# Kernel optimization log

Hardware: AMD Instinct MI355X
Metric: run time of the kernel (lower is better)

Reference implementation:

```python
import jax, jax.numpy as jnp
import numpy as np
from jax import lax

# norse LIF/LI default parameters
DT = 0.001
TAU_SYN_INV = 200.0   # 1/5e-3
TAU_MEM_INV = 100.0   # 1/1e-2
V_TH = 1.0
V_LEAK = 0.0
V_RESET = 0.0
ALPHA = 100.0         # SuperSpike surrogate slope (method='super')
SEQ_LEN = 40          # LIFConstantCurrentEncoder(40)
SCALE = 50.0

@jax.custom_vjp
def heaviside(x):
    # forward: spike if x > 0; backward: SuperSpike surrogate
    return (x > 0).astype(x.dtype)

def _h_fwd(x):
    return (x > 0).astype(x.dtype), x

def _h_bwd(x, g):
    return (g / (ALPHA * jnp.abs(x) + 1.0) ** 2,)

heaviside.defvjp(_h_fwd, _h_bwd)

def constant_current_encode(current):
    # LIF membrane driven by a constant input current; emit spike train (T, B, F)
    def step(v, _):
        v = v + DT * TAU_MEM_INV * ((V_LEAK - v) + current)
        z = heaviside(v - V_TH)
        v = (1.0 - z) * v  # reset to zero on spike
        return v, z
    _, spikes = lax.scan(step, jnp.zeros_like(current), None, length=SEQ_LEN)
    return spikes

def setup_inputs() -> dict:
    key = jax.random.key(0)
    k1, k2, k3, k4 = jax.random.split(key, 4)
    batch, state_dim, hidden, out = 65536, 4, 128, 2
    x = jax.random.normal(k1, (batch, state_dim), jnp.float32)
    s_in = np.float32(np.sqrt(1.0 / (2 * state_dim)))
    s_hid = np.float32(np.sqrt(1.0 / hidden))
    w_in = jax.random.normal(k2, (hidden, 2 * state_dim), jnp.float32) * s_in   # LIFCell input weights
    w_rec = jax.random.normal(k3, (hidden, hidden), jnp.float32) * s_hid        # LIFCell recurrent weights
    w_out = jax.random.normal(k4, (out, hidden), jnp.float32) * s_hid           # LICell readout weights
    return {"x": x, "w_in": w_in, "w_rec": w_rec, "w_out": w_out}

def reference(x, w_in, w_rec, w_out):
    # encode positive / negative parts of the (scaled) observation into spikes
    x_pos = constant_current_encode(jax.nn.relu(SCALE * x))   # (T, B, 4)
    x_neg = constant_current_encode(jax.nn.relu(-SCALE * x))  # (T, B, 4)
    spikes = jnp.concatenate([x_pos, x_neg], axis=2)          # (T, B, 8)

    B = x.shape[0]
    H = w_in.shape[0]
    O = w_out.shape[0]
    z0 = jnp.zeros((B, H), x.dtype)
    v0 = jnp.zeros((B, H), x.dtype)
    i0 = jnp.zeros((B, H), x.dtype)
    vo0 = jnp.zeros((B, O), x.dtype)
    io0 = jnp.zeros((B, O), x.dtype)

    def step(carry, xt):
        z, v, i, vo, io = carry
        # --- LIFCell (recurrent spiking layer) ---
        i_dec = i - DT * TAU_SYN_INV * i
        v_dec = v + DT * TAU_MEM_INV * ((V_LEAK - v) + i)
        z_new = heaviside(v_dec - V_TH)
        v_new = (1.0 - z_new) * v_dec + z_new * V_RESET
        i_new = i_dec + xt @ w_in.T + z @ w_rec.T
        # dropout(p=0.5) is identity in eval mode
        # --- LICell (leaky-integrator readout) ---
        vo_new = vo + DT * TAU_MEM_INV * ((V_LEAK - vo) + io)
        io_new = io - DT * TAU_SYN_INV * io + z_new @ w_out.T
        return (z_new, v_new, i_new, vo_new, io_new), vo_new

    _, voltages = lax.scan(step, (z0, v0, i0, vo0, io0), spikes)  # (T, B, 2)
    m = jnp.max(voltages, axis=0)
    return jax.nn.softmax(m, axis=1)
```

## Files before the change

### kernel.cpp

```cpp
#include <hip/hip_runtime.h>


#pragma clang fp contract(off)

typedef float f32x4 __attribute__((ext_vector_type(4)));
typedef float f32x2 __attribute__((ext_vector_type(2)));
typedef short short8 __attribute__((ext_vector_type(8)));
typedef int int4v __attribute__((ext_vector_type(4)));

constexpr int TSTEPS = 40;

__device__ __forceinline__ unsigned rnbf(float f) {
    unsigned u = __float_as_uint(f);
    return (u + 0x7FFFu + ((u >> 16) & 1u)) & 0xFFFF0000u;
}

__device__ __forceinline__ void split2pair(float a, float b,
                                           unsigned& hi, unsigned& mi) {
    unsigned ha = rnbf(a), hb = rnbf(b);
    float ra = a - __uint_as_float(ha);
    float rb = b - __uint_as_float(hb);
    unsigned ma = rnbf(ra), mb = rnbf(rb);
    hi = (ha >> 16) | (hb & 0xFFFF0000u);
    mi = (ma >> 16) | (mb & 0xFFFF0000u);
}

__device__ __forceinline__ f32x4 mfma16(int4v a, int4v b, f32x4 c) {
    return __builtin_amdgcn_mfma_f32_16x16x32_bf16(
        __builtin_bit_cast(short8, a), __builtin_bit_cast(short8, b), c, 0, 0, 0);
}

template <int CTRL>
__device__ __forceinline__ float dpp_mov(float v) {
    return __int_as_float(
        __builtin_amdgcn_update_dpp(0, __float_as_int(v), CTRL, 0xF, 0xF, true));
}

__device__ __forceinline__ f32x2 lo2(f32x4 a) {
    return __builtin_shufflevector(a, a, 0, 1);
}
__device__ __forceinline__ f32x2 hi2(f32x4 a) {
    return __builtin_shufflevector(a, a, 2, 3);
}

__global__ __launch_bounds__(256, 3) void snn_kernel(
    const float* __restrict__ x,
    const float* __restrict__ w_in,
    const float* __restrict__ w_rec,
    const float* __restrict__ w_out,
    float* __restrict__ out)
{
    __shared__ char zraw[8192];
    __shared__ __align__(16) unsigned long long msk[TSTEPS][2];

    const int tid = threadIdx.x;
    const int l   = tid & 63;
    const int wv  = tid >> 6;
    const int cl  = l & 15;
    const int kg  = l >> 4;
    const int kb  = kg * 8;
    const int b0  = blockIdx.x * 16;
    const int Ns  = wv * 32;
    const int des = blockIdx.x & 3;

    const f32x2 P1  = {0.1f, 0.1f};
    const f32x2 P02 = {0.2f, 0.2f};

    int4v BrecHi[2][4], BrecMi[2][4];
#pragma unroll
    for (int t = 0; t < 2; ++t) {
        int n = Ns + t * 16 + cl;
#pragma unroll
        for (int kc = 0; kc < 4; ++kc) {
            const float* wp = w_rec + n * 128 + kc * 32 + kb;
            float4 wa = *reinterpret_cast<const float4*>(wp);
            float4 wb = *reinterpret_cast<const float4*>(wp + 4);
            float w8[8] = {wa.x, wa.y, wa.z, wa.w, wb.x, wb.y, wb.z, wb.w};
#pragma unroll
            for (int r = 0; r < 4; ++r) {
                unsigned h, m;
                split2pair(w8[2 * r], w8[2 * r + 1], h, m);
                BrecHi[t][kc][r] = (int)h;
                BrecMi[t][kc][r] = (int)m;
            }
        }
    }

    int4v BwinPk[2];
#pragma unroll
    for (int t = 0; t < 2; ++t) {
        int n = Ns + t * 16 + cl;
        float w8[8];
#pragma unroll
        for (int j = 0; j < 8; ++j)
            w8[j] = (kg < 2) ? w_in[n * 8 + j] : 0.0f;
#pragma unroll
        for (int r = 0; r < 4; ++r) {
            unsigned h, m;
            split2pair(w8[2 * r], w8[2 * r + 1], h, m);
            BwinPk[t][r] = (int)(kg == 0 ? h : (kg == 1 ? m : 0u));
        }
    }

    int4v Bwout[4];
    {
        int  ch   = cl & 1;
        int  part = (cl >> 1) & 1;
        bool act  = cl < 4;
#pragma unroll
        for (int kc = 0; kc < 4; ++kc) {
            float w8[8];
#pragma unroll
            for (int j = 0; j < 8; ++j)
                w8[j] = act ? w_out[ch * 128 + kc * 32 + kb + j] : 0.0f;
#pragma unroll
            for (int r = 0; r < 4; ++r) {
                unsigned h, m;
                split2pair(w8[2 * r], w8[2 * r + 1], h, m);
                Bwout[kc][r] = (int)(part ? m : h);
            }
        }
    }

    if (wv == des) {
        float xv0 = x[(size_t)(b0 + (l >> 3)) * 4 + (l & 3)];
        float xv1 = x[(size_t)(b0 + 8 + (l >> 3)) * 4 + (l & 3)];
        float s0 = 50.0f * xv0, s1 = 50.0f * xv1;
        f32x2 cur, ve = {0.0f, 0.0f};
        cur[0] = (l & 4) ? fmaxf(-s0, 0.0f) : fmaxf(s0, 0.0f);
        cur[1] = (l & 4) ? fmaxf(-s1, 0.0f) : fmaxf(s1, 0.0f);
#pragma unroll 1
        for (int u = 0; u < TSTEPS; ++u) {
            f32x2 te = cur - ve;
            f32x2 vv = ve + P1 * te;
            bool e0 = vv[0] > 1.0f, e1 = vv[1] > 1.0f;
            unsigned long long bm0 = __ballot(e0), bm1 = __ballot(e1);
            ve[0] = e0 ? 0.0f : vv[0];
            ve[1] = e1 ? 0.0f : vv[1];
            if (l == 0) { msk[u][0] = bm0; msk[u][1] = bm1; }
        }
    }

    f32x2 iSl[2] = {{0,0},{0,0}}, iSh[2] = {{0,0},{0,0}};
    f32x2 vSl[2] = {{0,0},{0,0}}, vSh[2] = {{0,0},{0,0}};
    f32x2 io_l = {0,0}, io_h = {0,0}, vo_l = {0,0}, vo_h = {0,0};
    f32x4 mx = {-3e38f,-3e38f,-3e38f,-3e38f};

    unsigned awrb[2];
#pragma unroll
    for (int t = 0; t < 2; ++t) {
        int col = Ns + t * 16 + cl;
        awrb[t] = (unsigned)((kg * 1024 + col * 2) ^ ((kg & 1) << 6));
    }
    unsigned ard = (unsigned)((cl * 256 + kg * 16) ^ ((cl & 7) << 4)) | 4096u;

    auto loadfrags = [&](int4v* zf) {
#pragma unroll
        for (int kc = 0; kc < 4; ++kc)
            zf[kc] = *reinterpret_cast<int4v*>(&zraw[ard ^ (unsigned)(kc << 6)]);
    };

    auto readout = [&](const int4v* zf) {
        f32x4 cro = {0,0,0,0};
#pragma unroll
        for (int kc = 0; kc < 4; ++kc) cro = mfma16(zf[kc], Bwout[kc], cro);
        f32x4 cr;
#pragma unroll
        for (int r = 0; r < 4; ++r) cr[r] = cro[r] + dpp_mov<0x4E>(cro[r]);
        f32x2 t2l = io_l - vo_l;
        f32x2 t2h = io_h - vo_h;
        f32x2 vnl = vo_l + P1 * t2l;
        f32x2 vnh = vo_h + P1 * t2h;
        io_l = (io_l - P02 * io_l) + lo2(cr);
        io_h = (io_h - P02 * io_h) + hi2(cr);
        vo_l = vnl;
        vo_h = vnh;
        mx[0] = fmaxf(mx[0], vnl[0]);
        mx[1] = fmaxf(mx[1], vnl[1]);
        mx[2] = fmaxf(mx[2], vnh[0]);
        mx[3] = fmaxf(mx[3], vnh[1]);
    };

    auto encoder_lif = [&](int u, bool with_rec, const int4v* zf) {
        unsigned long long bm0 = msk[u][0];
        unsigned long long bm1 = msk[u][1];
        unsigned long long src = (cl < 8) ? (bm0 >> (cl * 8)) : (bm1 >> ((cl - 8) * 8));
        unsigned byt = (l < 32) ? ((unsigned)src & 0xFFu) : 0u;
        int4v axt;
        axt[0] = (int)(((byt & 1u)   ? 0x3F80u : 0u) | ((byt & 2u)   ? 0x3F800000u : 0u));
        axt[1] = (int)(((byt & 4u)   ? 0x3F80u : 0u) | ((byt & 8u)   ? 0x3F800000u : 0u));
        axt[2] = (int)(((byt & 16u)  ? 0x3F80u : 0u) | ((byt & 32u)  ? 0x3F800000u : 0u));
        axt[3] = (int)(((byt & 64u)  ? 0x3F80u : 0u) | ((byt & 128u) ? 0x3F800000u : 0u));
#pragma unroll
        for (int t = 0; t < 2; ++t) {
            f32x2 idl, idh, ttl, tth, vdl, vdh;
            f32x4 cin = {0,0,0,0};
            cin = mfma16(axt, BwinPk[t], cin);
            f32x4 crec = {0,0,0,0};
            if (with_rec) {
#pragma unroll
                for (int kc = 0; kc < 4; ++kc)
                    crec = mfma16(zf[kc], BrecMi[t][kc], crec);
#pragma unroll
                for (int kc = 0; kc < 4; ++kc)
                    crec = mfma16(zf[kc], BrecHi[t][kc], crec);
            }
            idl = iSl[t] - P02 * iSl[t];
            idh = iSh[t] - P02 * iSh[t];
            ttl = iSl[t] - vSl[t];
            tth = iSh[t] - vSh[t];
            vdl = vSl[t] + P1 * ttl;
            vdh = vSh[t] + P1 * tth;
#pragma unroll
            for (int r = 0; r < 4; ++r) {
                float vdr = (r < 2) ? vdl[r] : vdh[r - 2];
                bool zb = vdr > 1.0f;
                float vres = zb ? 0.0f : vdr;
                if (r == 0)      vSl[t][0] = vres;
                else if (r == 1) vSl[t][1] = vres;
                else if (r == 2) vSh[t][0] = vres;
                else             vSh[t][1] = vres;
                short zv = zb ? (short)0x3F80 : (short)0;
                unsigned a = (awrb[t] ^ (unsigned)(r << 4)) + (unsigned)(r * 256);
                *reinterpret_cast<short*>(&zraw[a]) = zv;
            }
            iSl[t] = (idl + lo2(cin)) + lo2(crec);
            iSh[t] = (idh + hi2(cin)) + hi2(crec);
        }
    };

    auto toggle = [&]() {
        ard ^= 4096u;
        awrb[0] ^= 4096u;
        awrb[1] ^= 4096u;
    };

    __syncthreads();
    encoder_lif(0, false, nullptr);
    __syncthreads();
    toggle();

#pragma unroll 1
    for (int u = 1; u < TSTEPS; ++u) {
        int4v zf[4];
        loadfrags(zf);
        if (wv == des) readout(zf);
        encoder_lif(u, true, zf);
        __syncthreads();
        toggle();
    }

    if (wv == des) {
        int4v zf[4];
        loadfrags(zf);
        readout(zf);
#pragma unroll
        for (int r = 0; r < 4; ++r) {
            float partner = dpp_mov<0xB1>(mx[r]);
            float mm = fmaxf(mx[r], partner);
            float es = expf(mx[r] - mm);
            float ep = expf(partner - mm);
            float inv = 1.0f / (es + ep);
            float pr = es * inv;
            if (cl < 2) out[(size_t)(b0 + kg * 4 + r) * 2 + cl] = pr;
        }
    }
}

extern "C" void kernel_launch(void* const* d_in, const int* in_sizes, int n_in,
                              void* d_out, int out_size, void* d_ws, size_t ws_size,
                              hipStream_t stream) {
    const float* x     = (const float*)d_in[0];
    const float* w_in  = (const float*)d_in[1];
    const float* w_rec = (const float*)d_in[2];
    const float* w_out = (const float*)d_in[3];
    float* out = (float*)d_out;

    int B = in_sizes[0] / 4;
    int blocks = B / 16;
    snn_kernel<<<blocks, 256, 0, stream>>>(x, w_in, w_rec, w_out, out);
}
```

Baseline: 245.4 us.

## Split hidden units across eight waves and stage readout weights in LDS

Blocks now launch 512 threads (eight waves) instead of four. Each wave owns 16 hidden neurons instead of 32, which halves the per-wave MFMA chain and register footprint per timestep. The readout weight fragments are moved from registers into shared memory and reloaded each step. The encoder is pinned to wave 1 and the weight staging to wave 0. The cost is more waves taking part in each per-step __syncthreads barrier and extra LDS traffic for the readout weights.

```diff
diff --git a/kernel.cpp b/kernel.cpp
--- a/kernel.cpp
+++ b/kernel.cpp
@@ -43,7 +43,7 @@
     return __builtin_shufflevector(a, a, 2, 3);
 }
 
-__global__ __launch_bounds__(256, 3) void snn_kernel(
+__global__ __launch_bounds__(512, 4) void snn_kernel(
     const float* __restrict__ x,
     const float* __restrict__ w_in,
     const float* __restrict__ w_rec,
@@ -51,6 +51,7 @@
     float* __restrict__ out)
 {
     __shared__ char zraw[8192];
+    __shared__ char woutlds[4096];
     __shared__ __align__(16) unsigned long long msk[TSTEPS][2];
 
     const int tid = threadIdx.x;
@@ -60,69 +61,64 @@
     const int kg  = l >> 4;
     const int kb  = kg * 8;
     const int b0  = blockIdx.x * 16;
-    const int Ns  = wv * 32;
-    const int des = blockIdx.x & 3;
+    const int n   = wv * 16 + cl;
+    const int des = blockIdx.x & 7;
 
     const f32x2 P1  = {0.1f, 0.1f};
     const f32x2 P02 = {0.2f, 0.2f};
 
-    int4v BrecHi[2][4], BrecMi[2][4];
-#pragma unroll
-    for (int t = 0; t < 2; ++t) {
-        int n = Ns + t * 16 + cl;
+    int4v BrecHi[4], BrecMi[4];
+#pragma unroll
+    for (int kc = 0; kc < 4; ++kc) {
+        const float* wp = w_rec + n * 128 + kc * 32 + kb;
+        float4 wa = *reinterpret_cast<const float4*>(wp);
+        float4 wb = *reinterpret_cast<const float4*>(wp + 4);
+        float w8[8] = {wa.x, wa.y, wa.z, wa.w, wb.x, wb.y, wb.z, wb.w};
+#pragma unroll
+        for (int r = 0; r < 4; ++r) {
+            unsigned h, m;
+            split2pair(w8[2 * r], w8[2 * r + 1], h, m);
+            BrecHi[kc][r] = (int)h;
+            BrecMi[kc][r] = (int)m;
+        }
+    }
+
+    int4v BwinPk;
+    {
+        float w8[8];
+#pragma unroll
+        for (int j = 0; j < 8; ++j)
+            w8[j] = (kg < 2) ? w_in[n * 8 + j] : 0.0f;
+#pragma unroll
+        for (int r = 0; r < 4; ++r) {
+            unsigned h, m;
+            split2pair(w8[2 * r], w8[2 * r + 1], h, m);
+            BwinPk[r] = (int)(kg == 0 ? h : (kg == 1 ? m : 0u));
+        }
+    }
+
+    if (wv == 0) {
+        int  ch   = cl & 1;
+        int  part = (cl >> 1) & 1;
+        bool act  = cl < 4;
 #pragma unroll
         for (int kc = 0; kc < 4; ++kc) {
-            const float* wp = w_rec + n * 128 + kc * 32 + kb;
-            float4 wa = *reinterpret_cast<const float4*>(wp);
-            float4 wb = *reinterpret_cast<const float4*>(wp + 4);
-            float w8[8] = {wa.x, wa.y, wa.z, wa.w, wb.x, wb.y, wb.z, wb.w};
+            float w8[8];
+#pragma unroll
+            for (int j = 0; j < 8; ++j)
+                w8[j] = act ? w_out[ch * 128 + kc * 32 + kb + j] : 0.0f;
+            int4v f;
 #pragma unroll
             for (int r = 0; r < 4; ++r) {
                 unsigned h, m;
                 split2pair(w8[2 * r], w8[2 * r + 1], h, m);
-                BrecHi[t][kc][r] = (int)h;
-                BrecMi[t][kc][r] = (int)m;
+                f[r] = (int)(part ? m : h);
             }
-        }
-    }
-
-    int4v BwinPk[2];
-#pragma unroll
-    for (int t = 0; t < 2; ++t) {
-        int n = Ns + t * 16 + cl;
-        float w8[8];
-#pragma unroll
-        for (int j = 0; j < 8; ++j)
-            w8[j] = (kg < 2) ? w_in[n * 8 + j] : 0.0f;
-#pragma unroll
-        for (int r = 0; r < 4; ++r) {
-            unsigned h, m;
-            split2pair(w8[2 * r], w8[2 * r + 1], h, m);
-            BwinPk[t][r] = (int)(kg == 0 ? h : (kg == 1 ? m : 0u));
-        }
-    }
-
-    int4v Bwout[4];
-    {
-        int  ch   = cl & 1;
-        int  part = (cl >> 1) & 1;
-        bool act  = cl < 4;
-#pragma unroll
-        for (int kc = 0; kc < 4; ++kc) {
-            float w8[8];
-#pragma unroll
-            for (int j = 0; j < 8; ++j)
-                w8[j] = act ? w_out[ch * 128 + kc * 32 + kb + j] : 0.0f;
-#pragma unroll
-            for (int r = 0; r < 4; ++r) {
-                unsigned h, m;
-                split2pair(w8[2 * r], w8[2 * r + 1], h, m);
-                Bwout[kc][r] = (int)(part ? m : h);
-            }
-        }
-    }
-
-    if (wv == des) {
+            *reinterpret_cast<int4v*>(&woutlds[kc * 1024 + l * 16]) = f;
+        }
+    }
+
+    if (wv == 1) {
         float xv0 = x[(size_t)(b0 + (l >> 3)) * 4 + (l & 3)];
         float xv1 = x[(size_t)(b0 + 8 + (l >> 3)) * 4 + (l & 3)];
         float s0 = 50.0f * xv0, s1 = 50.0f * xv1;
@@ -141,18 +137,12 @@
         }
     }
 
-    f32x2 iSl[2] = {{0,0},{0,0}}, iSh[2] = {{0,0},{0,0}};
-    f32x2 vSl[2] = {{0,0},{0,0}}, vSh[2] = {{0,0},{0,0}};
+    f32x2 iSl = {0,0}, iSh = {0,0}, vSl = {0,0}, vSh = {0,0};
     f32x2 io_l = {0,0}, io_h = {0,0}, vo_l = {0,0}, vo_h = {0,0};
     f32x4 mx = {-3e38f,-3e38f,-3e38f,-3e38f};
 
-    unsigned awrb[2];
-#pragma unroll
-    for (int t = 0; t < 2; ++t) {
-        int col = Ns + t * 16 + cl;
-        awrb[t] = (unsigned)((kg * 1024 + col * 2) ^ ((kg & 1) << 6));
-    }
-    unsigned ard = (unsigned)((cl * 256 + kg * 16) ^ ((cl & 7) << 4)) | 4096u;
+    unsigned awrb = (unsigned)((kg * 1024 + n * 2) ^ ((kg & 1) << 6));
+    unsigned ard  = (unsigned)((cl * 256 + kg * 16) ^ ((cl & 7) << 4)) | 4096u;
 
     auto loadfrags = [&](int4v* zf) {
 #pragma unroll
@@ -161,9 +151,13 @@
     };
 
     auto readout = [&](const int4v* zf) {
+        int4v bw[4];
+#pragma unroll
+        for (int kc = 0; kc < 4; ++kc)
+            bw[kc] = *reinterpret_cast<int4v*>(&woutlds[kc * 1024 + l * 16]);
         f32x4 cro = {0,0,0,0};
 #pragma unroll
-        for (int kc = 0; kc < 4; ++kc) cro = mfma16(zf[kc], Bwout[kc], cro);
+        for (int kc = 0; kc < 4; ++kc) cro = mfma16(zf[kc], bw[kc], cro);
         f32x4 cr;
 #pragma unroll
         for (int r = 0; r < 4; ++r) cr[r] = cro[r] + dpp_mov<0x4E>(cro[r]);
@@ -191,48 +185,43 @@
         axt[1] = (int)(((byt & 4u)   ? 0x3F80u : 0u) | ((byt & 8u)   ? 0x3F800000u : 0u));
         axt[2] = (int)(((byt & 16u)  ? 0x3F80u : 0u) | ((byt & 32u)  ? 0x3F800000u : 0u));
         axt[3] = (int)(((byt & 64u)  ? 0x3F80u : 0u) | ((byt & 128u) ? 0x3F800000u : 0u));
-#pragma unroll
-        for (int t = 0; t < 2; ++t) {
-            f32x2 idl, idh, ttl, tth, vdl, vdh;
-            f32x4 cin = {0,0,0,0};
-            cin = mfma16(axt, BwinPk[t], cin);
-            f32x4 crec = {0,0,0,0};
-            if (with_rec) {
-#pragma unroll
-                for (int kc = 0; kc < 4; ++kc)
-                    crec = mfma16(zf[kc], BrecMi[t][kc], crec);
-#pragma unroll
-                for (int kc = 0; kc < 4; ++kc)
-                    crec = mfma16(zf[kc], BrecHi[t][kc], crec);
-            }
-            idl = iSl[t] - P02 * iSl[t];
-            idh = iSh[t] - P02 * iSh[t];
-            ttl = iSl[t] - vSl[t];
-            tth = iSh[t] - vSh[t];
-            vdl = vSl[t] + P1 * ttl;
-            vdh = vSh[t] + P1 * tth;
-#pragma unroll
-            for (int r = 0; r < 4; ++r) {
-                float vdr = (r < 2) ? vdl[r] : vdh[r - 2];
-                bool zb = vdr > 1.0f;
-                float vres = zb ? 0.0f : vdr;
-                if (r == 0)      vSl[t][0] = vres;
-                else if (r == 1) vSl[t][1] = vres;
-                else if (r == 2) vSh[t][0] = vres;
-                else             vSh[t][1] = vres;
-                short zv = zb ? (short)0x3F80 : (short)0;
-                unsigned a = (awrb[t] ^ (unsigned)(r << 4)) + (unsigned)(r * 256);
-                *reinterpret_cast<short*>(&zraw[a]) = zv;
-            }
-            iSl[t] = (idl + lo2(cin)) + lo2(crec);
-            iSh[t] = (idh + hi2(cin)) + hi2(crec);
-        }
+        f32x4 cin = {0,0,0,0};
+        cin = mfma16(axt, BwinPk, cin);
+        f32x4 crec = {0,0,0,0};
+        if (with_rec) {
+#pragma unroll
+            for (int kc = 0; kc < 4; ++kc)
+                crec = mfma16(zf[kc], BrecMi[kc], crec);
+#pragma unroll
+            for (int kc = 0; kc < 4; ++kc)
+                crec = mfma16(zf[kc], BrecHi[kc], crec);
+        }
+        f32x2 idl = iSl - P02 * iSl;
+        f32x2 idh = iSh - P02 * iSh;
+        f32x2 ttl = iSl - vSl;
+        f32x2 tth = iSh - vSh;
+        f32x2 vdl = vSl + P1 * ttl;
+        f32x2 vdh = vSh + P1 * tth;
+#pragma unroll
+        for (int r = 0; r < 4; ++r) {
+            float vdr = (r < 2) ? vdl[r] : vdh[r - 2];
+            bool zb = vdr > 1.0f;
+            float vres = zb ? 0.0f : vdr;
+            if (r == 0)      vSl[0] = vres;
+            else if (r == 1) vSl[1] = vres;
+            else if (r == 2) vSh[0] = vres;
+            else             vSh[1] = vres;
+            short zv = zb ? (short)0x3F80 : (short)0;
+            unsigned a = (awrb ^ (unsigned)(r << 4)) + (unsigned)(r * 256);
+            *reinterpret_cast<short*>(&zraw[a]) = zv;
+        }
+        iSl = (idl + lo2(cin)) + lo2(crec);
+        iSh = (idh + hi2(cin)) + hi2(crec);
     };
 
     auto toggle = [&]() {
-        ard ^= 4096u;
-        awrb[0] ^= 4096u;
-        awrb[1] ^= 4096u;
+        ard  ^= 4096u;
+        awrb ^= 4096u;
     };
 
     __syncthreads();
@@ -278,5 +267,5 @@
 
     int B = in_sizes[0] / 4;
     int blocks = B / 16;
-    snn_kernel<<<blocks, 256, 0, stream>>>(x, w_in, w_rec, w_out, out);
-}
+    snn_kernel<<<blocks, 512, 0, stream>>>(x, w_in, w_rec, w_out, out);
+}
```

After: 325.6 us. 32.7% more time.

## Precompute encoder spike fragments in LDS and rotate readout MFMA across waves

Applied to the files above, without the earlier changes.

The encoder wave now builds the packed bf16 input-spike MFMA fragments once per timestep and stores them in LDS, so each wave's step only loads a 16-byte vector instead of decoding ballot masks. The readout matmul is rotated across the four waves by timestep and writes its per-step currents to LDS. The serial LI integration and max then run once at the end on a single wave. This spreads the extra readout work evenly so no single wave lengthens every step, at the cost of about 25 KB more LDS, which may reduce occupancy.

```diff
diff --git a/kernel.cpp b/kernel.cpp
--- a/kernel.cpp
+++ b/kernel.cpp
@@ -50,8 +50,9 @@
     const float* __restrict__ w_out,
     float* __restrict__ out)
 {
-    __shared__ char zraw[8192];
-    __shared__ __align__(16) unsigned long long msk[TSTEPS][2];
+    __shared__ __align__(16) char zraw[8192];
+    __shared__ __align__(16) char axtlds[TSTEPS * 512];
+    __shared__ float crlds[TSTEPS][16][2];
 
     const int tid = threadIdx.x;
     const int l   = tid & 63;
@@ -137,14 +138,21 @@
             unsigned long long bm0 = __ballot(e0), bm1 = __ballot(e1);
             ve[0] = e0 ? 0.0f : vv[0];
             ve[1] = e1 ? 0.0f : vv[1];
-            if (l == 0) { msk[u][0] = bm0; msk[u][1] = bm1; }
+            unsigned long long src = (cl < 8) ? (bm0 >> (cl * 8))
+                                              : (bm1 >> ((cl - 8) * 8));
+            unsigned byt = (unsigned)src & 0xFFu;
+            int4v axt;
+            axt[0] = (int)(((byt & 1u)   ? 0x3F80u : 0u) | ((byt & 2u)   ? 0x3F800000u : 0u));
+            axt[1] = (int)(((byt & 4u)   ? 0x3F80u : 0u) | ((byt & 8u)   ? 0x3F800000u : 0u));
+            axt[2] = (int)(((byt & 16u)  ? 0x3F80u : 0u) | ((byt & 32u)  ? 0x3F800000u : 0u));
+            axt[3] = (int)(((byt & 64u)  ? 0x3F80u : 0u) | ((byt & 128u) ? 0x3F800000u : 0u));
+            if (l < 32)
+                *reinterpret_cast<int4v*>(&axtlds[u * 512 + l * 16]) = axt;
         }
     }
 
     f32x2 iSl[2] = {{0,0},{0,0}}, iSh[2] = {{0,0},{0,0}};
     f32x2 vSl[2] = {{0,0},{0,0}}, vSh[2] = {{0,0},{0,0}};
-    f32x2 io_l = {0,0}, io_h = {0,0}, vo_l = {0,0}, vo_h = {0,0};
-    f32x4 mx = {-3e38f,-3e38f,-3e38f,-3e38f};
 
     unsigned awrb[2];
 #pragma unroll
@@ -160,40 +168,24 @@
             zf[kc] = *reinterpret_cast<int4v*>(&zraw[ard ^ (unsigned)(kc << 6)]);
     };
 
-    auto readout = [&](const int4v* zf) {
+    auto readout_cr = [&](const int4v* zf, int slot) {
         f32x4 cro = {0,0,0,0};
 #pragma unroll
         for (int kc = 0; kc < 4; ++kc) cro = mfma16(zf[kc], Bwout[kc], cro);
         f32x4 cr;
 #pragma unroll
         for (int r = 0; r < 4; ++r) cr[r] = cro[r] + dpp_mov<0x4E>(cro[r]);
-        f32x2 t2l = io_l - vo_l;
-        f32x2 t2h = io_h - vo_h;
-        f32x2 vnl = vo_l + P1 * t2l;
-        f32x2 vnh = vo_h + P1 * t2h;
-        io_l = (io_l - P02 * io_l) + lo2(cr);
-        io_h = (io_h - P02 * io_h) + hi2(cr);
-        vo_l = vnl;
-        vo_h = vnh;
-        mx[0] = fmaxf(mx[0], vnl[0]);
-        mx[1] = fmaxf(mx[1], vnl[1]);
-        mx[2] = fmaxf(mx[2], vnh[0]);
-        mx[3] = fmaxf(mx[3], vnh[1]);
+        if (cl < 2) {
+#pragma unroll
+            for (int r = 0; r < 4; ++r) crlds[slot][kg * 4 + r][cl] = cr[r];
+        }
     };
 
     auto encoder_lif = [&](int u, bool with_rec, const int4v* zf) {
-        unsigned long long bm0 = msk[u][0];
-        unsigned long long bm1 = msk[u][1];
-        unsigned long long src = (cl < 8) ? (bm0 >> (cl * 8)) : (bm1 >> ((cl - 8) * 8));
-        unsigned byt = (l < 32) ? ((unsigned)src & 0xFFu) : 0u;
-        int4v axt;
-        axt[0] = (int)(((byt & 1u)   ? 0x3F80u : 0u) | ((byt & 2u)   ? 0x3F800000u : 0u));
-        axt[1] = (int)(((byt & 4u)   ? 0x3F80u : 0u) | ((byt & 8u)   ? 0x3F800000u : 0u));
-        axt[2] = (int)(((byt & 16u)  ? 0x3F80u : 0u) | ((byt & 32u)  ? 0x3F800000u : 0u));
-        axt[3] = (int)(((byt & 64u)  ? 0x3F80u : 0u) | ((byt & 128u) ? 0x3F800000u : 0u));
+        int4v axt = *reinterpret_cast<const int4v*>(
+            &axtlds[u * 512 + (l & 31) * 16]);
 #pragma unroll
         for (int t = 0; t < 2; ++t) {
-            f32x2 idl, idh, ttl, tth, vdl, vdh;
             f32x4 cin = {0,0,0,0};
             cin = mfma16(axt, BwinPk[t], cin);
             f32x4 crec = {0,0,0,0};
@@ -205,12 +197,12 @@
                 for (int kc = 0; kc < 4; ++kc)
                     crec = mfma16(zf[kc], BrecHi[t][kc], crec);
             }
-            idl = iSl[t] - P02 * iSl[t];
-            idh = iSh[t] - P02 * iSh[t];
-            ttl = iSl[t] - vSl[t];
-            tth = iSh[t] - vSh[t];
-            vdl = vSl[t] + P1 * ttl;
-            vdh = vSh[t] + P1 * tth;
+            f32x2 idl = iSl[t] - P02 * iSl[t];
+            f32x2 idh = iSh[t] - P02 * iSh[t];
+            f32x2 ttl = iSl[t] - vSl[t];
+            f32x2 tth = iSh[t] - vSh[t];
+            f32x2 vdl = vSl[t] + P1 * ttl;
+            f32x2 vdh = vSh[t] + P1 * tth;
 #pragma unroll
             for (int r = 0; r < 4; ++r) {
                 float vdr = (r < 2) ? vdl[r] : vdh[r - 2];
@@ -244,7 +236,7 @@
     for (int u = 1; u < TSTEPS; ++u) {
         int4v zf[4];
         loadfrags(zf);
-        if (wv == des) readout(zf);
+        if (wv == (u & 3)) readout_cr(zf, u - 1);
         encoder_lif(u, true, zf);
         __syncthreads();
         toggle();
@@ -253,7 +245,28 @@
     if (wv == des) {
         int4v zf[4];
         loadfrags(zf);
-        readout(zf);
+        readout_cr(zf, TSTEPS - 1);
+        f32x4 io = {0,0,0,0}, vo = {0,0,0,0};
+        f32x4 mx = {-3e38f,-3e38f,-3e38f,-3e38f};
+        const int ch = cl & 1;
+#pragma unroll 1
+        for (int u = 0; u < TSTEPS; ++u) {
+            f32x4 cr4;
+#pragma unroll
+            for (int r = 0; r < 4; ++r) cr4[r] = crlds[u][kg * 4 + r][ch];
+            f32x4 vn;
+#pragma unroll
+            for (int r = 0; r < 4; ++r) {
+                float t2 = io[r] - vo[r];
+                vn[r] = vo[r] + 0.1f * t2;
+            }
+#pragma unroll
+            for (int r = 0; r < 4; ++r)
+                io[r] = (io[r] - 0.2f * io[r]) + cr4[r];
+            vo = vn;
+#pragma unroll
+            for (int r = 0; r < 4; ++r) mx[r] = fmaxf(mx[r], vn[r]);
+        }
 #pragma unroll
         for (int r = 0; r < 4; ++r) {
             float partner = dpp_mov<0xB1>(mx[r]);
```

Result: no change. 240.7 us (-1.9%).
